# Kernel optimization log

Measured on AMD Instinct MI355X. Metric: run time of the kernel, lower is better.

## Reference

```python
import jax, jax.numpy as jnp
import numpy as np

TAU = 20.0        # LIFNeuron default tau
THRESHOLD = 1.0   # LIFNeuron default threshold
RESET = 0.0       # LIFNeuron default reset
DT = 1.0          # SpikingNeuralNetwork dt
ALPHA = DT / TAU

B, T, I, H, O = 256, 128, 512, 1024, 512


def setup_inputs() -> dict:
    key = jax.random.key(0)
    ks = jax.random.split(key, 6)
    def w(k, shape, fan_in):
        return (jax.random.normal(k, shape, jnp.float32) / np.sqrt(fan_in)).astype(jnp.float32)
    return {
        "x":  jax.random.normal(ks[0], (B, T, I), jnp.float32),
        "We": w(ks[1], (I, H), I), "be": jnp.zeros((H,), jnp.float32),
        "W1": w(ks[2], (H, H), H), "b1": jnp.zeros((H,), jnp.float32),
        "W2": w(ks[3], (H, H), H), "b2": jnp.zeros((H,), jnp.float32),
        "Wo": w(ks[4], (H, O), H), "bo": jnp.zeros((O,), jnp.float32),
    }


def _lif(v, inp):
    # v += (-v + inp) * dt/tau; spike = (v >= thr); v = v*(1-spike) + reset*spike
    v = v + (inp - v) * ALPHA
    spike = (v >= THRESHOLD).astype(v.dtype)
    v = v * (1.0 - spike) + RESET * spike
    return v, spike


def reference(x, We, be, W1, b1, W2, b2, Wo, bo):
    b, t, _ = x.shape
    h_dim = We.shape[1]
    o_dim = Wo.shape[1]

    def step(carry, xt):
        v1, v2, vo = carry
        h = jax.nn.relu(xt @ We + be)          # [B, H]
        v1, s1 = _lif(v1, h)                   # neuron 0 (only 2 of 3 neurons used: zip truncation)
        h = s1 @ W1 + b1
        v2, s2 = _lif(v2, h)                   # neuron 1
        h = s2 @ W2 + b2                       # last hidden layer: no neuron applied before output_layer
        vo, so = _lif(vo, h @ Wo + bo)         # output neuron
        return (v1, v2, vo), (s1, s2, so)

    init = (jnp.zeros((b, h_dim), x.dtype),
            jnp.zeros((b, h_dim), x.dtype),
            jnp.zeros((b, o_dim), x.dtype))
    _, (S1, S2, SO) = jax.lax.scan(step, init, jnp.swapaxes(x, 0, 1))  # time-major scan
    # output_spike at last timestep + full (detached) spike history, stacked over time
    return SO[-1], S1, S2, SO
```

## Files before the change

### kernel.cpp

```cpp
#include <hip/hip_runtime.h>
#include <cstdint>
#include <cstddef>

#define B_ 256
#define T_ 128
#define I_ 512
#define H_ 1024
#define O_ 512
static constexpr float ALPHA = 1.0f / 20.0f;
static constexpr float THR   = 1.0f;
static constexpr float S12   = 0.000244140625f;

typedef _Float16 f16;
typedef __attribute__((ext_vector_type(8))) _Float16 f16x8;
typedef __attribute__((ext_vector_type(4))) float f32x4;

template<bool PERM_X, bool RELU>
__global__ __launch_bounds__(256)
void gemm128(const float* __restrict__ A, const float* __restrict__ Bw,
             const float* __restrict__ bias, float* __restrict__ C,
             int M, int N, int K) {
    constexpr int BM = 128, BN = 128, BK = 16, TM = 8, TN = 8;
    __shared__ float As[BK][BM];
    __shared__ float Bs[BK][BN + 4];

    const int tid = threadIdx.x;
    const int ntile = N / BN;
    const int bx = blockIdx.x % ntile;
    const int by = blockIdx.x / ntile;
    const int row0 = by * BM, col0 = bx * BN;
    const int tx = tid & 15;
    const int ty = tid >> 4;

    float acc[TM][TN] = {};

    for (int k0 = 0; k0 < K; k0 += BK) {
#pragma unroll
        for (int p = 0; p < 2; ++p) {
            int f = tid + p * 256;
            int r  = f >> 2;
            int kc = (f & 3) << 2;
            int m = row0 + r;
            const float* arow;
            if (PERM_X) {
                int t = m >> 8;
                int b = m & 255;
                arow = A + (size_t)(b * T_ + t) * K;
            } else {
                arow = A + (size_t)m * K;
            }
            float4 v = *reinterpret_cast<const float4*>(arow + k0 + kc);
            As[kc + 0][r] = v.x;
            As[kc + 1][r] = v.y;
            As[kc + 2][r] = v.z;
            As[kc + 3][r] = v.w;
        }
#pragma unroll
        for (int p = 0; p < 2; ++p) {
            int f = tid + p * 256;
            int r  = f >> 5;
            int nc = (f & 31) << 2;
            float4 v = *reinterpret_cast<const float4*>(Bw + (size_t)(k0 + r) * N + col0 + nc);
            *reinterpret_cast<float4*>(&Bs[r][nc]) = v;
        }
        __syncthreads();

#pragma unroll
        for (int k = 0; k < BK; ++k) {
            float a[TM], b[TN];
#pragma unroll
            for (int i = 0; i < TM; ++i) a[i] = As[k][ty * TM + i];
#pragma unroll
            for (int j = 0; j < TN; ++j) b[j] = Bs[k][tx * TN + j];
#pragma unroll
            for (int i = 0; i < TM; ++i)
#pragma unroll
                for (int j = 0; j < TN; ++j)
                    acc[i][j] += a[i] * b[j];
        }
        __syncthreads();
    }

#pragma unroll
    for (int i = 0; i < TM; ++i) {
        size_t m = (size_t)(row0 + ty * TM + i);
#pragma unroll
        for (int jj = 0; jj < TN; jj += 4) {
            int n = col0 + tx * TN + jj;
            float4 c4;
            float c0 = acc[i][jj + 0] + bias[n + 0];
            float c1 = acc[i][jj + 1] + bias[n + 1];
            float c2 = acc[i][jj + 2] + bias[n + 2];
            float c3 = acc[i][jj + 3] + bias[n + 3];
            if (RELU) {
                c0 = fmaxf(c0, 0.f); c1 = fmaxf(c1, 0.f);
                c2 = fmaxf(c2, 0.f); c3 = fmaxf(c3, 0.f);
            }
            c4.x = c0; c4.y = c1; c4.z = c2; c4.w = c3;
            *reinterpret_cast<float4*>(C + m * N + n) = c4;
        }
    }
}

__device__ inline void gload_lds16(const void* gsrc, void* ldsdst) {
    __builtin_amdgcn_global_load_lds(
        (const __attribute__((address_space(1))) unsigned int*)gsrc,
        (__attribute__((address_space(3))) unsigned int*)ldsdst, 16, 0, 0);
}

template<bool SPLITX, bool PERM, bool RELU, bool WRITE_LAST>
__global__ __launch_bounds__(256, 2)
void gemm_lif(const float* __restrict__ A,
              const f16* __restrict__ Bhi,
              const f16* __restrict__ Blo,
              const float* __restrict__ bias,
              float* __restrict__ S,
              float* __restrict__ last_out,
              int N, int K) {
    constexpr int BK = 32;
    constexpr int NBUF = SPLITX ? 4 : 3;
    constexpr int BUFSTR = NBUF * 4096;
    constexpr size_t SMEM = (2 * BUFSTR * 2 > 64 * 132 * 4)
                                ? (size_t)(2 * BUFSTR * 2)
                                : (size_t)(64 * 132 * 4);
    __shared__ __align__(16) char smem[SMEM];
    f16* sm = (f16*)smem;
    float (*Cs)[132] = (float (*)[132])smem;

    const int tid  = threadIdx.x;
    const int lane = tid & 63;
    const int w    = tid >> 6;
    const int wr   = w >> 1, wc = w & 1;
    const int ntile = N >> 7;
    const int bx = blockIdx.x % ntile;
    const int b  = blockIdx.x / ntile;
    const int col0 = bx << 7;

    f32x4 acc0[4][4], acc1[4][4];
#pragma unroll
    for (int mi = 0; mi < 4; ++mi)
#pragma unroll
        for (int ni = 0; ni < 4; ++ni) {
            acc0[mi][ni] = {0.f, 0.f, 0.f, 0.f};
            acc1[mi][ni] = {0.f, 0.f, 0.f, 0.f};
        }

    {
        f16* Ah0 = sm;
        f16* Bh0 = sm + 4096;
        f16* Bl0 = sm + 8192;
        f16* Al0 = sm + 12288;
#pragma unroll
        for (int p = 0; p < 2; ++p) {
            int chunk = w * 2 + p;
            int r  = chunk * 16 + (lane >> 2);
            int kq = lane & 3;
            size_t off = (size_t)(col0 + r) * K + kq * 8;
            gload_lds16(Bhi + off, Bh0 + chunk * 512);
            gload_lds16(Blo + off, Bl0 + chunk * 512);
        }
#pragma unroll
        for (int p = 0; p < 4; ++p) {
            int c = tid + p * 256;
            int r = c >> 3;
            int q = c & 7;
            const float* arow = PERM ? A + (size_t)(b * T_ + r) * K
                                     : A + (size_t)(r * B_ + b) * K;
            float4 v = *reinterpret_cast<const float4*>(arow + q * 4);
            union { f16 h[4]; uint2 u; } hi;
            hi.h[0] = (f16)v.x; hi.h[1] = (f16)v.y;
            hi.h[2] = (f16)v.z; hi.h[3] = (f16)v.w;
            *reinterpret_cast<uint2*>(&Ah0[r * BK + q * 4]) = hi.u;
            if (SPLITX) {
                union { f16 h[4]; uint2 u; } lo;
                lo.h[0] = (f16)((v.x - (float)hi.h[0]) * 4096.0f);
                lo.h[1] = (f16)((v.y - (float)hi.h[1]) * 4096.0f);
                lo.h[2] = (f16)((v.z - (float)hi.h[2]) * 4096.0f);
                lo.h[3] = (f16)((v.w - (float)hi.h[3]) * 4096.0f);
                *reinterpret_cast<uint2*>(&Al0[r * BK + q * 4]) = lo.u;
            }
        }
    }
    __syncthreads();

    const int NIT = K / BK;
    for (int it = 0; it < NIT; ++it) {
        const int cur = it & 1, nxt = cur ^ 1;
        const bool more = (it + 1 < NIT);
        const int k0n = (it + 1) * BK;

        f16* Ah_c = sm + cur * BUFSTR;
        f16* Bh_c = Ah_c + 4096;
        f16* Bl_c = Ah_c + 8192;
        f16* Al_c = Ah_c + 12288;
        f16* Ah_n = sm + nxt * BUFSTR;
        f16* Bh_n = Ah_n + 4096;
        f16* Bl_n = Ah_n + 8192;
        f16* Al_n = Ah_n + 12288;

        float4 a4[4];
        if (more) {
#pragma unroll
            for (int p = 0; p < 2; ++p) {
                int chunk = w * 2 + p;
                int r  = chunk * 16 + (lane >> 2);
                int kq = lane & 3;
                size_t off = (size_t)(col0 + r) * K + k0n + kq * 8;
                gload_lds16(Bhi + off, Bh_n + chunk * 512);
                gload_lds16(Blo + off, Bl_n + chunk * 512);
            }
#pragma unroll
            for (int p = 0; p < 4; ++p) {
                int c = tid + p * 256;
                int r = c >> 3;
                int q = c & 7;
                const float* arow = PERM ? A + (size_t)(b * T_ + r) * K
                                         : A + (size_t)(r * B_ + b) * K;
                a4[p] = *reinterpret_cast<const float4*>(arow + k0n + q * 4);
            }
        }

        {
            f16x8 ahi[4], alo[4];
#pragma unroll
            for (int mi = 0; mi < 4; ++mi) {
                int ar = (wr * 64 + mi * 16 + (lane & 15)) * BK + (lane >> 4) * 8;
                ahi[mi] = *reinterpret_cast<const f16x8*>(&Ah_c[ar]);
                if (SPLITX) alo[mi] = *reinterpret_cast<const f16x8*>(&Al_c[ar]);
            }
#pragma unroll
            for (int ni = 0; ni < 4; ++ni) {
                int br = (wc * 64 + ni * 16 + (lane & 15)) * BK + (lane >> 4) * 8;
                f16x8 bh = *reinterpret_cast<const f16x8*>(&Bh_c[br]);
                f16x8 bl = *reinterpret_cast<const f16x8*>(&Bl_c[br]);
#pragma unroll
                for (int mi = 0; mi < 4; ++mi) {
                    acc0[mi][ni] = __builtin_amdgcn_mfma_f32_16x16x32_f16(
                        ahi[mi], bh, acc0[mi][ni], 0, 0, 0);
                    acc1[mi][ni] = __builtin_amdgcn_mfma_f32_16x16x32_f16(
                        ahi[mi], bl, acc1[mi][ni], 0, 0, 0);
                    if (SPLITX)
                        acc1[mi][ni] = __builtin_amdgcn_mfma_f32_16x16x32_f16(
                            alo[mi], bh, acc1[mi][ni], 0, 0, 0);
                }
            }
        }

        if (more) {
#pragma unroll
            for (int p = 0; p < 4; ++p) {
                int c = tid + p * 256;
                int r = c >> 3;
                int q = c & 7;
                float4 v = a4[p];
                union { f16 h[4]; uint2 u; } hi;
                hi.h[0] = (f16)v.x; hi.h[1] = (f16)v.y;
                hi.h[2] = (f16)v.z; hi.h[3] = (f16)v.w;
                *reinterpret_cast<uint2*>(&Ah_n[r * BK + q * 4]) = hi.u;
                if (SPLITX) {
                    union { f16 h[4]; uint2 u; } lo;
                    lo.h[0] = (f16)((v.x - (float)hi.h[0]) * 4096.0f);
                    lo.h[1] = (f16)((v.y - (float)hi.h[1]) * 4096.0f);
                    lo.h[2] = (f16)((v.z - (float)hi.h[2]) * 4096.0f);
                    lo.h[3] = (f16)((v.w - (float)hi.h[3]) * 4096.0f);
                    *reinterpret_cast<uint2*>(&Al_n[r * BK + q * 4]) = lo.u;
                }
            }
        }
        __syncthreads();
    }

    float v = 0.f, s = 0.f;
    float* Sp = S + (size_t)b * N + col0 + (tid & 127);
    const size_t tstride = (size_t)B_ * N;

    if (wr == 0) {
#pragma unroll
        for (int ni = 0; ni < 4; ++ni) {
            int col = wc * 64 + ni * 16 + (lane & 15);
            float bv = bias[col0 + col];
#pragma unroll
            for (int mi = 0; mi < 4; ++mi) {
                int rowb = mi * 16 + ((lane >> 4) << 2);
#pragma unroll
                for (int r = 0; r < 4; ++r) {
                    float cv = acc0[mi][ni][r] + S12 * acc1[mi][ni][r] + bv;
                    if (RELU) cv = fmaxf(cv, 0.f);
                    Cs[rowb + r][col] = cv;
                }
            }
        }
    }
    __syncthreads();
    if (tid < 128) {
#pragma unroll 4
        for (int t = 0; t < 64; ++t) {
            float in = Cs[t][tid];
            v = v + (in - v) * ALPHA;
            bool sp = (v >= THR);
            s = sp ? 1.0f : 0.0f;
            Sp[(size_t)t * tstride] = s;
            v = sp ? 0.0f : v;
        }
    }
    __syncthreads();
    if (wr == 1) {
#pragma unroll
        for (int ni = 0; ni < 4; ++ni) {
            int col = wc * 64 + ni * 16 + (lane & 15);
            float bv = bias[col0 + col];
#pragma unroll
            for (int mi = 0; mi < 4; ++mi) {
                int rowb = mi * 16 + ((lane >> 4) << 2);
#pragma unroll
                for (int r = 0; r < 4; ++r) {
                    float cv = acc0[mi][ni][r] + S12 * acc1[mi][ni][r] + bv;
                    if (RELU) cv = fmaxf(cv, 0.f);
                    Cs[rowb + r][col] = cv;
                }
            }
        }
    }
    __syncthreads();
    if (tid < 128) {
#pragma unroll 4
        for (int t = 64; t < 128; ++t) {
            float in = Cs[t - 64][tid];
            v = v + (in - v) * ALPHA;
            bool sp = (v >= THR);
            s = sp ? 1.0f : 0.0f;
            Sp[(size_t)t * tstride] = s;
            v = sp ? 0.0f : v;
        }
        if (WRITE_LAST) last_out[(size_t)b * N + col0 + tid] = s;
    }
}

__global__ __launch_bounds__(256)
void lif_scan(float* __restrict__ buf, int BH, float* __restrict__ last_out) {
    int j = blockIdx.x * 256 + threadIdx.x;
    if (j >= BH) return;
    float v = 0.f;
    float last = 0.f;
    for (int t = 0; t < T_; ++t) {
        size_t idx = (size_t)t * BH + j;
        float in = buf[idx];
        v = v + (in - v) * ALPHA;
        bool sp = (v >= THR);
        last = sp ? 1.0f : 0.0f;
        buf[idx] = last;
        v = sp ? 0.0f : v;
    }
    if (last_out) last_out[j] = last;
}

__global__ __launch_bounds__(256)
void make_wf2(const float* __restrict__ W2, const float* __restrict__ Wo,
              float* __restrict__ Wf) {
    __shared__ float w2s[64][33];
    __shared__ float wos[64][68];
    const int tid = threadIdx.x;
    const int ht = blockIdx.x >> 3, ot = blockIdx.x & 7;
    const int h0 = ht * 32, o0 = ot * 64;
    const int th = tid >> 3;
    const int to = tid & 7;

    double acc[8] = {0, 0, 0, 0, 0, 0, 0, 0};

    for (int k0 = 0; k0 < H_; k0 += 64) {
#pragma unroll
        for (int p = 0; p < 2; ++p) {
            int f = tid + p * 256;
            int i = f >> 4;
            int j4 = (f & 15) << 2;
            float4 v = *reinterpret_cast<const float4*>(
                W2 + (size_t)(h0 + i) * H_ + k0 + j4);
            w2s[j4 + 0][i] = v.x; w2s[j4 + 1][i] = v.y;
            w2s[j4 + 2][i] = v.z; w2s[j4 + 3][i] = v.w;
        }
#pragma unroll
        for (int p = 0; p < 4; ++p) {
            int f = tid + p * 256;
            int r = f >> 4;
            int c4 = (f & 15) << 2;
            float4 v = *reinterpret_cast<const float4*>(
                Wo + (size_t)(k0 + r) * O_ + o0 + c4);
            wos[r][c4 + 0] = v.x; wos[r][c4 + 1] = v.y;
            wos[r][c4 + 2] = v.z; wos[r][c4 + 3] = v.w;
        }
        __syncthreads();

#pragma unroll 8
        for (int k = 0; k < 64; ++k) {
            double a = (double)w2s[k][th];
#pragma unroll
            for (int j = 0; j < 8; ++j)
                acc[j] += a * (double)wos[k][to * 8 + j];
        }
        __syncthreads();
    }
#pragma unroll
    for (int j = 0; j < 8; ++j)
        Wf[(size_t)(h0 + th) * O_ + o0 + to * 8 + j] = (float)acc[j];
}

__global__ __launch_bounds__(256)
void make_bf(const float* __restrict__ Wo, const float* __restrict__ b2,
             const float* __restrict__ bo, float* __restrict__ bf) {
    int o = blockIdx.x * 256 + threadIdx.x;
    if (o >= O_) return;
    double acc = (double)bo[o];
    for (int h = 0; h < H_; ++h)
        acc += (double)b2[h] * (double)Wo[(size_t)h * O_ + o];
    bf[o] = (float)acc;
}

__global__ __launch_bounds__(256)
void split_w16(const float* __restrict__ W, f16* __restrict__ hi,
               f16* __restrict__ lo, int K, int N) {
    int idx = blockIdx.x * 256 + threadIdx.x;
    if (idx >= K * N) return;
    int n = idx / K;
    int k = idx - n * K;
    float wv = W[(size_t)k * N + n];
    f16 h0 = (f16)wv;
    float r = (wv - (float)h0) * 4096.0f;
    f16 h1 = (f16)r;
    hi[idx] = h0; lo[idx] = h1;
}

extern "C" void kernel_launch(void* const* d_in, const int* in_sizes, int n_in,
                              void* d_out, int out_size, void* d_ws, size_t ws_size,
                              hipStream_t stream) {
    const float* x  = (const float*)d_in[0];
    const float* We = (const float*)d_in[1];
    const float* be = (const float*)d_in[2];
    const float* W1 = (const float*)d_in[3];
    const float* b1 = (const float*)d_in[4];
    const float* W2 = (const float*)d_in[5];
    const float* b2 = (const float*)d_in[6];
    const float* Wo = (const float*)d_in[7];
    const float* bo = (const float*)d_in[8];

    float* out = (float*)d_out;
    float* so_last = out;
    float* S1 = out + (size_t)B_ * O_;
    float* S2 = S1 + (size_t)T_ * B_ * H_;
    float* SO = S2 + (size_t)T_ * B_ * H_;

    const int TB = T_ * B_;
    dim3 blk(256);

    const size_t sz_we  = (size_t)I_ * H_ * 2;
    const size_t sz_w1  = (size_t)H_ * H_ * 2;
    const size_t sz_wf  = (size_t)H_ * O_ * 2;
    const size_t off_weh = 0;
    const size_t off_wel = off_weh + sz_we;
    const size_t off_w1h = off_wel + sz_we;
    const size_t off_w1l = off_w1h + sz_w1;
    const size_t off_wf32 = off_w1l + sz_w1;
    const size_t off_bf   = off_wf32 + (size_t)H_ * O_ * 4;
    const size_t off_wfh  = off_bf + (size_t)O_ * 4;
    const size_t off_wfl  = off_wfh + sz_wf;
    const size_t need     = off_wfl + sz_wf;

    if (ws_size >= need) {
        char* ws = (char*)d_ws;
        f16*   weh = (f16*)(ws + off_weh);
        f16*   wel = (f16*)(ws + off_wel);
        f16*   w1h = (f16*)(ws + off_w1h);
        f16*   w1l = (f16*)(ws + off_w1l);
        float* Wf  = (float*)(ws + off_wf32);
        float* bf  = (float*)(ws + off_bf);
        f16*   wfh = (f16*)(ws + off_wfh);
        f16*   wfl = (f16*)(ws + off_wfl);

        split_w16<<<dim3((I_ * H_ + 255) / 256), blk, 0, stream>>>(We, weh, wel, I_, H_);
        split_w16<<<dim3((H_ * H_ + 255) / 256), blk, 0, stream>>>(W1, w1h, w1l, H_, H_);
        make_wf2<<<dim3(256), blk, 0, stream>>>(W2, Wo, Wf);
        make_bf<<<dim3(2), blk, 0, stream>>>(Wo, b2, bo, bf);
        split_w16<<<dim3((H_ * O_ + 255) / 256), blk, 0, stream>>>(Wf, wfh, wfl, H_, O_);

        gemm_lif<true, true, true, false><<<dim3(B_ * (H_ / 128)), blk, 0, stream>>>(
            x, weh, wel, be, S1, nullptr, H_, I_);

        gemm_lif<false, false, false, false><<<dim3(B_ * (H_ / 128)), blk, 0, stream>>>(
            S1, w1h, w1l, b1, S2, nullptr, H_, H_);

        gemm_lif<false, false, false, true><<<dim3(B_ * (O_ / 128)), blk, 0, stream>>>(
            S2, wfh, wfl, bf, SO, so_last, O_, H_);
    } else {
        float* Wf = (float*)d_ws;
        float* bf = Wf + (size_t)H_ * O_;
        gemm128<true, true><<<dim3((TB / 128) * (H_ / 128)), blk, 0, stream>>>(
            x, We, be, S1, TB, H_, I_);
        lif_scan<<<dim3((B_ * H_ + 255) / 256), blk, 0, stream>>>(S1, B_ * H_, nullptr);
        gemm128<false, false><<<dim3((TB / 128) * (H_ / 128)), blk, 0, stream>>>(
            S1, W1, b1, S2, TB, H_, H_);
        lif_scan<<<dim3((B_ * H_ + 255) / 256), blk, 0, stream>>>(S2, B_ * H_, nullptr);
        make_wf2<<<dim3(256), blk, 0, stream>>>(W2, Wo, Wf);
        make_bf<<<dim3(2), blk, 0, stream>>>(Wo, b2, bo, bf);
        gemm128<false, false><<<dim3((TB / 128) * (O_ / 128)), blk, 0, stream>>>(
            S2, Wf, bf, SO, TB, O_, H_);
        lif_scan<<<dim3((B_ * O_ + 255) / 256), blk, 0, stream>>>(SO, B_ * O_, so_last);
    }
}
```

Measured before the change: 644.3 us.

## Pack spike outputs into bitmasks and feed packed spikes to later GEMMs

The first and second LIF GEMM kernels now also write each timestep's spikes as ballot bitmasks into a packed workspace buffer. The following GEMM reads these 1-bit spikes and expands them to f16 in registers instead of loading fp32 spike tensors, and it drops the low-part A MFMA because spikes are exactly 0/1 in f16. Weight splits are pre-swizzled so direct global-to-LDS loads land in a bank-conflict-free layout, and blocks are remapped to group batches. This adds extra ballot stores and more workspace use, and the new path is taken only when the workspace is large enough.

```diff
diff --git a/kernel.cpp b/kernel.cpp
--- a/kernel.cpp
+++ b/kernel.cpp
@@ -14,6 +14,12 @@
 typedef _Float16 f16;
 typedef __attribute__((ext_vector_type(8))) _Float16 f16x8;
 typedef __attribute__((ext_vector_type(4))) float f32x4;
+
+__device__ inline void gload_lds16(const void* gsrc, void* ldsdst) {
+    __builtin_amdgcn_global_load_lds(
+        (const __attribute__((address_space(1))) unsigned int*)gsrc,
+        (__attribute__((address_space(3))) unsigned int*)ldsdst, 16, 0, 0);
+}
 
 template<bool PERM_X, bool RELU>
 __global__ __launch_bounds__(256)
@@ -102,20 +108,12 @@
     }
 }
 
-__device__ inline void gload_lds16(const void* gsrc, void* ldsdst) {
-    __builtin_amdgcn_global_load_lds(
-        (const __attribute__((address_space(1))) unsigned int*)gsrc,
-        (__attribute__((address_space(3))) unsigned int*)ldsdst, 16, 0, 0);
-}
-
 template<bool SPLITX, bool PERM, bool RELU, bool WRITE_LAST>
 __global__ __launch_bounds__(256, 2)
 void gemm_lif(const float* __restrict__ A,
-              const f16* __restrict__ Bhi,
-              const f16* __restrict__ Blo,
+              const f16* __restrict__ Bhi, const f16* __restrict__ Blo,
               const float* __restrict__ bias,
-              float* __restrict__ S,
-              float* __restrict__ last_out,
+              float* __restrict__ S, float* __restrict__ last_out,
               int N, int K) {
     constexpr int BK = 32;
     constexpr int NBUF = SPLITX ? 4 : 3;
@@ -336,6 +334,408 @@
     }
 }
 
+__global__ __launch_bounds__(256, 2)
+void gemm_lif_x(const float* __restrict__ A,
+                const f16* __restrict__ Bhi, const f16* __restrict__ Blo,
+                const float* __restrict__ bias,
+                float* __restrict__ S,
+                uint32_t* __restrict__ Pk,
+                int N, int K) {
+    constexpr int BK = 32;
+    constexpr int BUFSTR = 4 * 4096;
+    __shared__ __align__(16) char smem[2 * BUFSTR * 2];
+    f16* sm = (f16*)smem;
+    float (*Cs)[132] = (float (*)[132])smem;
+
+    const int tid  = threadIdx.x;
+    const int lane = tid & 63;
+    const int w    = tid >> 6;
+    const int wr   = w >> 1, wc = w & 1;
+    const int nt   = N >> 7;
+    const int ls   = 31 - __builtin_clz(nt);
+    const int jj_  = blockIdx.x >> 3;
+    const int bx   = jj_ & (nt - 1);
+    const int b    = ((blockIdx.x & 7) << 5) + (jj_ >> ls);
+    const int col0 = bx << 7;
+    const int sw = (((lane >> 4) ^ ((lane >> 1) & 3)) << 3);
+
+    f32x4 acc0[4][4], acc1[4][4];
+#pragma unroll
+    for (int mi = 0; mi < 4; ++mi)
+#pragma unroll
+        for (int ni = 0; ni < 4; ++ni) {
+            acc0[mi][ni] = {0.f, 0.f, 0.f, 0.f};
+            acc1[mi][ni] = {0.f, 0.f, 0.f, 0.f};
+        }
+
+    {
+        f16* Ah0 = sm;
+        f16* Bh0 = sm + 4096;
+        f16* Bl0 = sm + 8192;
+        f16* Al0 = sm + 12288;
+#pragma unroll
+        for (int p = 0; p < 2; ++p) {
+            int chunk = w * 2 + p;
+            int r  = chunk * 16 + (lane >> 2);
+            int kq = lane & 3;
+            size_t off = (size_t)(col0 + r) * K + kq * 8;
+            gload_lds16(Bhi + off, Bh0 + chunk * 512);
+            gload_lds16(Blo + off, Bl0 + chunk * 512);
+        }
+#pragma unroll
+        for (int p = 0; p < 4; ++p) {
+            int c = tid + p * 256;
+            int r = c >> 3;
+            int q = c & 7;
+            const float* arow = A + (size_t)(b * T_ + r) * K;
+            float4 v = *reinterpret_cast<const float4*>(arow + q * 4);
+            int aoff = r * 32 + ((((q >> 1) ^ ((r >> 1) & 3))) << 3) + ((q & 1) << 2);
+            union { f16 h[4]; uint2 u; } hi;
+            hi.h[0] = (f16)v.x; hi.h[1] = (f16)v.y;
+            hi.h[2] = (f16)v.z; hi.h[3] = (f16)v.w;
+            *reinterpret_cast<uint2*>(&Ah0[aoff]) = hi.u;
+            union { f16 h[4]; uint2 u; } lo;
+            lo.h[0] = (f16)((v.x - (float)hi.h[0]) * 4096.0f);
+            lo.h[1] = (f16)((v.y - (float)hi.h[1]) * 4096.0f);
+            lo.h[2] = (f16)((v.z - (float)hi.h[2]) * 4096.0f);
+            lo.h[3] = (f16)((v.w - (float)hi.h[3]) * 4096.0f);
+            *reinterpret_cast<uint2*>(&Al0[aoff]) = lo.u;
+        }
+    }
+    __syncthreads();
+
+    const int NIT = K / BK;
+    for (int it = 0; it < NIT; ++it) {
+        const int cur = it & 1, nxt = cur ^ 1;
+        const bool more = (it + 1 < NIT);
+        const int k0n = (it + 1) * BK;
+
+        f16* Ah_c = sm + cur * BUFSTR;
+        f16* Bh_c = Ah_c + 4096;
+        f16* Bl_c = Ah_c + 8192;
+        f16* Al_c = Ah_c + 12288;
+        f16* Ah_n = sm + nxt * BUFSTR;
+        f16* Bh_n = Ah_n + 4096;
+        f16* Bl_n = Ah_n + 8192;
+        f16* Al_n = Ah_n + 12288;
+
+        float4 a4[4];
+        if (more) {
+#pragma unroll
+            for (int p = 0; p < 2; ++p) {
+                int chunk = w * 2 + p;
+                int r  = chunk * 16 + (lane >> 2);
+                int kq = lane & 3;
+                size_t off = (size_t)(col0 + r) * K + k0n + kq * 8;
+                gload_lds16(Bhi + off, Bh_n + chunk * 512);
+                gload_lds16(Blo + off, Bl_n + chunk * 512);
+            }
+#pragma unroll
+            for (int p = 0; p < 4; ++p) {
+                int c = tid + p * 256;
+                int r = c >> 3;
+                int q = c & 7;
+                const float* arow = A + (size_t)(b * T_ + r) * K;
+                a4[p] = *reinterpret_cast<const float4*>(arow + k0n + q * 4);
+            }
+        }
+
+        {
+            f16x8 ahi[4], alo[4];
+#pragma unroll
+            for (int mi = 0; mi < 4; ++mi) {
+                int ar = (wr * 64 + mi * 16 + (lane & 15)) * 32 + sw;
+                ahi[mi] = *reinterpret_cast<const f16x8*>(&Ah_c[ar]);
+                alo[mi] = *reinterpret_cast<const f16x8*>(&Al_c[ar]);
+            }
+#pragma unroll
+            for (int ni = 0; ni < 4; ++ni) {
+                int br = (wc * 64 + ni * 16 + (lane & 15)) * 32 + sw;
+                f16x8 bh = *reinterpret_cast<const f16x8*>(&Bh_c[br]);
+                f16x8 bl = *reinterpret_cast<const f16x8*>(&Bl_c[br]);
+#pragma unroll
+                for (int mi = 0; mi < 4; ++mi) {
+                    acc0[mi][ni] = __builtin_amdgcn_mfma_f32_16x16x32_f16(
+                        ahi[mi], bh, acc0[mi][ni], 0, 0, 0);
+                    acc1[mi][ni] = __builtin_amdgcn_mfma_f32_16x16x32_f16(
+                        ahi[mi], bl, acc1[mi][ni], 0, 0, 0);
+                    acc1[mi][ni] = __builtin_amdgcn_mfma_f32_16x16x32_f16(
+                        alo[mi], bh, acc1[mi][ni], 0, 0, 0);
+                }
+            }
+        }
+
+        if (more) {
+#pragma unroll
+            for (int p = 0; p < 4; ++p) {
+                int c = tid + p * 256;
+                int r = c >> 3;
+                int q = c & 7;
+                float4 v = a4[p];
+                int aoff = r * 32 + ((((q >> 1) ^ ((r >> 1) & 3))) << 3) + ((q & 1) << 2);
+                union { f16 h[4]; uint2 u; } hi;
+                hi.h[0] = (f16)v.x; hi.h[1] = (f16)v.y;
+                hi.h[2] = (f16)v.z; hi.h[3] = (f16)v.w;
+                *reinterpret_cast<uint2*>(&Ah_n[aoff]) = hi.u;
+                union { f16 h[4]; uint2 u; } lo;
+                lo.h[0] = (f16)((v.x - (float)hi.h[0]) * 4096.0f);
+                lo.h[1] = (f16)((v.y - (float)hi.h[1]) * 4096.0f);
+                lo.h[2] = (f16)((v.z - (float)hi.h[2]) * 4096.0f);
+                lo.h[3] = (f16)((v.w - (float)hi.h[3]) * 4096.0f);
+                *reinterpret_cast<uint2*>(&Al_n[aoff]) = lo.u;
+            }
+        }
+        __syncthreads();
+    }
+
+    float v = 0.f;
+    float* Sp = S + (size_t)b * N + col0 + (tid & 127);
+    const size_t tstride = (size_t)B_ * N;
+    const int PkW = N >> 5;
+    const size_t pkbase = (size_t)(col0 >> 5) + ((tid >> 6) << 1);
+
+    if (wr == 0) {
+#pragma unroll
+        for (int ni = 0; ni < 4; ++ni) {
+            int col = wc * 64 + ni * 16 + (lane & 15);
+            float bv = bias[col0 + col];
+#pragma unroll
+            for (int mi = 0; mi < 4; ++mi) {
+                int rowb = mi * 16 + ((lane >> 4) << 2);
+#pragma unroll
+                for (int r = 0; r < 4; ++r) {
+                    float cv = fmaxf(acc0[mi][ni][r] + S12 * acc1[mi][ni][r] + bv, 0.f);
+                    Cs[rowb + r][col] = cv;
+                }
+            }
+        }
+    }
+    __syncthreads();
+    if (tid < 128) {
+#pragma unroll 4
+        for (int t = 0; t < 64; ++t) {
+            float in = Cs[t][tid];
+            v = v + (in - v) * ALPHA;
+            bool sp = (v >= THR);
+            Sp[(size_t)t * tstride] = sp ? 1.0f : 0.0f;
+            v = sp ? 0.0f : v;
+            unsigned long long bm = __ballot(sp);
+            if (lane == 0)
+                *reinterpret_cast<unsigned long long*>(
+                    &Pk[((size_t)t * B_ + b) * PkW + pkbase]) = bm;
+        }
+    }
+    __syncthreads();
+    if (wr == 1) {
+#pragma unroll
+        for (int ni = 0; ni < 4; ++ni) {
+            int col = wc * 64 + ni * 16 + (lane & 15);
+            float bv = bias[col0 + col];
+#pragma unroll
+            for (int mi = 0; mi < 4; ++mi) {
+                int rowb = mi * 16 + ((lane >> 4) << 2);
+#pragma unroll
+                for (int r = 0; r < 4; ++r) {
+                    float cv = fmaxf(acc0[mi][ni][r] + S12 * acc1[mi][ni][r] + bv, 0.f);
+                    Cs[rowb + r][col] = cv;
+                }
+            }
+        }
+    }
+    __syncthreads();
+    if (tid < 128) {
+#pragma unroll 4
+        for (int t = 64; t < 128; ++t) {
+            float in = Cs[t - 64][tid];
+            v = v + (in - v) * ALPHA;
+            bool sp = (v >= THR);
+            Sp[(size_t)t * tstride] = sp ? 1.0f : 0.0f;
+            v = sp ? 0.0f : v;
+            unsigned long long bm = __ballot(sp);
+            if (lane == 0)
+                *reinterpret_cast<unsigned long long*>(
+                    &Pk[((size_t)t * B_ + b) * PkW + pkbase]) = bm;
+        }
+    }
+}
+
+template<bool WRITE_LAST, bool PACK_OUT>
+__global__ __launch_bounds__(256, 2)
+void gemm_lif_pk(const uint32_t* __restrict__ Apk,
+                 const f16* __restrict__ Bhi, const f16* __restrict__ Blo,
+                 const float* __restrict__ bias,
+                 float* __restrict__ S,
+                 float* __restrict__ last_out,
+                 uint32_t* __restrict__ Pk_out,
+                 int N, int K) {
+    __shared__ __align__(16) char smem[64 * 132 * 4];
+    f16* sm = (f16*)smem;
+    float (*Cs)[132] = (float (*)[132])smem;
+
+    const int tid  = threadIdx.x;
+    const int lane = tid & 63;
+    const int w    = tid >> 6;
+    const int wr   = w >> 1, wc = w & 1;
+    const int nt   = N >> 7;
+    const int ls   = 31 - __builtin_clz(nt);
+    const int jj_  = blockIdx.x >> 3;
+    const int bx   = jj_ & (nt - 1);
+    const int b    = ((blockIdx.x & 7) << 5) + (jj_ >> ls);
+    const int col0 = bx << 7;
+    const int sw = (((lane >> 4) ^ ((lane >> 1) & 3)) << 3);
+    const int PkW = K >> 5;
+    const int sh  = (lane >> 4) << 3;
+
+    size_t arow[4];
+#pragma unroll
+    for (int mi = 0; mi < 4; ++mi) {
+        int r = wr * 64 + mi * 16 + (lane & 15);
+        arow[mi] = ((size_t)r * B_ + b) * PkW;
+    }
+
+    f32x4 acc0[4][4], acc1[4][4];
+#pragma unroll
+    for (int mi = 0; mi < 4; ++mi)
+#pragma unroll
+        for (int ni = 0; ni < 4; ++ni) {
+            acc0[mi][ni] = {0.f, 0.f, 0.f, 0.f};
+            acc1[mi][ni] = {0.f, 0.f, 0.f, 0.f};
+        }
+
+    {
+#pragma unroll
+        for (int p = 0; p < 2; ++p) {
+            int chunk = w * 2 + p;
+            int r  = chunk * 16 + (lane >> 2);
+            int kq = lane & 3;
+            size_t off = (size_t)(col0 + r) * K + kq * 8;
+            gload_lds16(Bhi + off, sm + chunk * 512);
+            gload_lds16(Blo + off, sm + 4096 + chunk * 512);
+        }
+    }
+    __syncthreads();
+
+    const int NIT = K / 32;
+    for (int it = 0; it < NIT; ++it) {
+        const int cur = it & 1, nxt = cur ^ 1;
+        f16* Bh_c = sm + cur * 8192;
+        f16* Bl_c = Bh_c + 4096;
+        if (it + 1 < NIT) {
+            f16* Bh_n = sm + nxt * 8192;
+            f16* Bl_n = Bh_n + 4096;
+            int k0n = (it + 1) * 32;
+#pragma unroll
+            for (int p = 0; p < 2; ++p) {
+                int chunk = w * 2 + p;
+                int r  = chunk * 16 + (lane >> 2);
+                int kq = lane & 3;
+                size_t off = (size_t)(col0 + r) * K + k0n + kq * 8;
+                gload_lds16(Bhi + off, Bh_n + chunk * 512);
+                gload_lds16(Blo + off, Bl_n + chunk * 512);
+            }
+        }
+
+        f16x8 af[4];
+#pragma unroll
+        for (int mi = 0; mi < 4; ++mi) {
+            uint32_t mm = Apk[arow[mi] + it] >> sh;
+            union { f16 h[8]; f16x8 v; } au;
+#pragma unroll
+            for (int j = 0; j < 8; ++j)
+                au.h[j] = ((mm >> j) & 1) ? (f16)1.0f : (f16)0.0f;
+            af[mi] = au.v;
+        }
+
+#pragma unroll
+        for (int ni = 0; ni < 4; ++ni) {
+            int br = (wc * 64 + ni * 16 + (lane & 15)) * 32 + sw;
+            f16x8 bh = *reinterpret_cast<const f16x8*>(&Bh_c[br]);
+            f16x8 bl = *reinterpret_cast<const f16x8*>(&Bl_c[br]);
+#pragma unroll
+            for (int mi = 0; mi < 4; ++mi) {
+                acc0[mi][ni] = __builtin_amdgcn_mfma_f32_16x16x32_f16(
+                    af[mi], bh, acc0[mi][ni], 0, 0, 0);
+                acc1[mi][ni] = __builtin_amdgcn_mfma_f32_16x16x32_f16(
+                    af[mi], bl, acc1[mi][ni], 0, 0, 0);
+            }
+        }
+        __syncthreads();
+    }
+
+    float v = 0.f, s = 0.f;
+    float* Sp = S + (size_t)b * N + col0 + (tid & 127);
+    const size_t tstride = (size_t)B_ * N;
+    const int PkWo = N >> 5;
+    const size_t pkbase = (size_t)(col0 >> 5) + ((tid >> 6) << 1);
+
+    if (wr == 0) {
+#pragma unroll
+        for (int ni = 0; ni < 4; ++ni) {
+            int col = wc * 64 + ni * 16 + (lane & 15);
+            float bv = bias[col0 + col];
+#pragma unroll
+            for (int mi = 0; mi < 4; ++mi) {
+                int rowb = mi * 16 + ((lane >> 4) << 2);
+#pragma unroll
+                for (int r = 0; r < 4; ++r)
+                    Cs[rowb + r][col] = acc0[mi][ni][r] + S12 * acc1[mi][ni][r] + bv;
+            }
+        }
+    }
+    __syncthreads();
+    if (tid < 128) {
+#pragma unroll 4
+        for (int t = 0; t < 64; ++t) {
+            float in = Cs[t][tid];
+            v = v + (in - v) * ALPHA;
+            bool sp = (v >= THR);
+            s = sp ? 1.0f : 0.0f;
+            Sp[(size_t)t * tstride] = s;
+            v = sp ? 0.0f : v;
+            if (PACK_OUT) {
+                unsigned long long bm = __ballot(sp);
+                if (lane == 0)
+                    *reinterpret_cast<unsigned long long*>(
+                        &Pk_out[((size_t)t * B_ + b) * PkWo + pkbase]) = bm;
+            }
+        }
+    }
+    __syncthreads();
+    if (wr == 1) {
+#pragma unroll
+        for (int ni = 0; ni < 4; ++ni) {
+            int col = wc * 64 + ni * 16 + (lane & 15);
+            float bv = bias[col0 + col];
+#pragma unroll
+            for (int mi = 0; mi < 4; ++mi) {
+                int rowb = mi * 16 + ((lane >> 4) << 2);
+#pragma unroll
+                for (int r = 0; r < 4; ++r)
+                    Cs[rowb + r][col] = acc0[mi][ni][r] + S12 * acc1[mi][ni][r] + bv;
+            }
+        }
+    }
+    __syncthreads();
+    if (tid < 128) {
+#pragma unroll 4
+        for (int t = 64; t < 128; ++t) {
+            float in = Cs[t - 64][tid];
+            v = v + (in - v) * ALPHA;
+            bool sp = (v >= THR);
+            s = sp ? 1.0f : 0.0f;
+            Sp[(size_t)t * tstride] = s;
+            v = sp ? 0.0f : v;
+            if (PACK_OUT) {
+                unsigned long long bm = __ballot(sp);
+                if (lane == 0)
+                    *reinterpret_cast<unsigned long long*>(
+                        &Pk_out[((size_t)t * B_ + b) * PkWo + pkbase]) = bm;
+            }
+        }
+        if (WRITE_LAST) last_out[(size_t)b * N + col0 + tid] = s;
+    }
+}
+
 __global__ __launch_bounds__(256)
 void lif_scan(float* __restrict__ buf, int BH, float* __restrict__ last_out) {
     int j = blockIdx.x * 256 + threadIdx.x;
@@ -415,13 +815,16 @@
     bf[o] = (float)acc;
 }
 
+template<bool SWZ>
 __global__ __launch_bounds__(256)
 void split_w16(const float* __restrict__ W, f16* __restrict__ hi,
                f16* __restrict__ lo, int K, int N) {
     int idx = blockIdx.x * 256 + threadIdx.x;
     if (idx >= K * N) return;
     int n = idx / K;
-    int k = idx - n * K;
+    int ks = idx - n * K;
+    int k = SWZ ? ((ks & ~31) | ((((ks >> 3) & 3) ^ ((n >> 1) & 3)) << 3) | (ks & 7))
+                : ks;
     float wv = W[(size_t)k * N + n];
     f16 h0 = (f16)wv;
     float r = (wv - (float)h0) * 4096.0f;
@@ -451,42 +854,76 @@
     const int TB = T_ * B_;
     dim3 blk(256);
 
-    const size_t sz_we  = (size_t)I_ * H_ * 2;
-    const size_t sz_w1  = (size_t)H_ * H_ * 2;
-    const size_t sz_wf  = (size_t)H_ * O_ * 2;
+    const size_t MB = 1024 * 1024;
     const size_t off_weh = 0;
-    const size_t off_wel = off_weh + sz_we;
-    const size_t off_w1h = off_wel + sz_we;
-    const size_t off_w1l = off_w1h + sz_w1;
-    const size_t off_wf32 = off_w1l + sz_w1;
-    const size_t off_bf   = off_wf32 + (size_t)H_ * O_ * 4;
-    const size_t off_wfh  = off_bf + (size_t)O_ * 4;
-    const size_t off_wfl  = off_wfh + sz_wf;
-    const size_t need     = off_wfl + sz_wf;
-
-    if (ws_size >= need) {
+    const size_t off_wel = 1 * MB;
+    const size_t off_w1h = 2 * MB;
+    const size_t off_w1l = 4 * MB;
+    const size_t off_wfh = 6 * MB;
+    const size_t off_wfl = 7 * MB;
+    const size_t off_bf  = 8 * MB;
+    const size_t off_D   = 8 * MB + 4096;
+    const size_t off_pk2 = off_D + 4 * MB;
+    const size_t need3   = off_pk2 + 4 * MB;
+
+    const size_t m_off_weh = 0;
+    const size_t m_off_wel = m_off_weh + (size_t)I_ * H_ * 2;
+    const size_t m_off_w1h = m_off_wel + (size_t)I_ * H_ * 2;
+    const size_t m_off_w1l = m_off_w1h + (size_t)H_ * H_ * 2;
+    const size_t m_off_wf32 = m_off_w1l + (size_t)H_ * H_ * 2;
+    const size_t m_off_bf   = m_off_wf32 + (size_t)H_ * O_ * 4;
+    const size_t m_off_wfh  = m_off_bf + (size_t)O_ * 4;
+    const size_t m_off_wfl  = m_off_wfh + (size_t)H_ * O_ * 2;
+    const size_t need2      = m_off_wfl + (size_t)H_ * O_ * 2;
+
+    if (ws_size >= need3) {
         char* ws = (char*)d_ws;
         f16*   weh = (f16*)(ws + off_weh);
         f16*   wel = (f16*)(ws + off_wel);
         f16*   w1h = (f16*)(ws + off_w1h);
         f16*   w1l = (f16*)(ws + off_w1l);
-        float* Wf  = (float*)(ws + off_wf32);
-        float* bf  = (float*)(ws + off_bf);
         f16*   wfh = (f16*)(ws + off_wfh);
         f16*   wfl = (f16*)(ws + off_wfl);
-
-        split_w16<<<dim3((I_ * H_ + 255) / 256), blk, 0, stream>>>(We, weh, wel, I_, H_);
-        split_w16<<<dim3((H_ * H_ + 255) / 256), blk, 0, stream>>>(W1, w1h, w1l, H_, H_);
+        float* bf  = (float*)(ws + off_bf);
+        float* Wf  = (float*)(ws + off_D);
+        uint32_t* pk1 = (uint32_t*)(ws + off_D);
+        uint32_t* pk2 = (uint32_t*)(ws + off_pk2);
+
+        split_w16<true><<<dim3((I_ * H_ + 255) / 256), blk, 0, stream>>>(We, weh, wel, I_, H_);
+        split_w16<true><<<dim3((H_ * H_ + 255) / 256), blk, 0, stream>>>(W1, w1h, w1l, H_, H_);
         make_wf2<<<dim3(256), blk, 0, stream>>>(W2, Wo, Wf);
         make_bf<<<dim3(2), blk, 0, stream>>>(Wo, b2, bo, bf);
-        split_w16<<<dim3((H_ * O_ + 255) / 256), blk, 0, stream>>>(Wf, wfh, wfl, H_, O_);
+        split_w16<true><<<dim3((H_ * O_ + 255) / 256), blk, 0, stream>>>(Wf, wfh, wfl, H_, O_);
+
+        gemm_lif_x<<<dim3(B_ * (H_ / 128)), blk, 0, stream>>>(
+            x, weh, wel, be, S1, pk1, H_, I_);
+
+        gemm_lif_pk<false, true><<<dim3(B_ * (H_ / 128)), blk, 0, stream>>>(
+            pk1, w1h, w1l, b1, S2, nullptr, pk2, H_, H_);
+
+        gemm_lif_pk<true, false><<<dim3(B_ * (O_ / 128)), blk, 0, stream>>>(
+            pk2, wfh, wfl, bf, SO, so_last, nullptr, O_, H_);
+    } else if (ws_size >= need2) {
+        char* ws = (char*)d_ws;
+        f16*   weh = (f16*)(ws + m_off_weh);
+        f16*   wel = (f16*)(ws + m_off_wel);
+        f16*   w1h = (f16*)(ws + m_off_w1h);
+        f16*   w1l = (f16*)(ws + m_off_w1l);
+        float* Wf  = (float*)(ws + m_off_wf32);
+        float* bf  = (float*)(ws + m_off_bf);
+        f16*   wfh = (f16*)(ws + m_off_wfh);
+        f16*   wfl = (f16*)(ws + m_off_wfl);
+
+        split_w16<false><<<dim3((I_ * H_ + 255) / 256), blk, 0, stream>>>(We, weh, wel, I_, H_);
+        split_w16<false><<<dim3((H_ * H_ + 255) / 256), blk, 0, stream>>>(W1, w1h, w1l, H_, H_);
+        make_wf2<<<dim3(256), blk, 0, stream>>>(W2, Wo, Wf);
+        make_bf<<<dim3(2), blk, 0, stream>>>(Wo, b2, bo, bf);
+        split_w16<false><<<dim3((H_ * O_ + 255) / 256), blk, 0, stream>>>(Wf, wfh, wfl, H_, O_);
 
         gemm_lif<true, true, true, false><<<dim3(B_ * (H_ / 128)), blk, 0, stream>>>(
             x, weh, wel, be, S1, nullptr, H_, I_);
-
         gemm_lif<false, false, false, false><<<dim3(B_ * (H_ / 128)), blk, 0, stream>>>(
             S1, w1h, w1l, b1, S2, nullptr, H_, H_);
-
         gemm_lif<false, false, false, true><<<dim3(B_ * (O_ / 128)), blk, 0, stream>>>(
             S2, wfh, wfl, bf, SO, so_last, O_, H_);
     } else {
```

New measurement: 657.0 us. No clear change (+2.0%).

## Emit f16 spike copies and consume them in dedicated f16-A GEMM-LIF kernels

Applied to the files above, without the earlier changes.

The first two GEMM-LIF stages now also write their spike outputs as f16 into a batch-major workspace buffer. A new gemm_lif_h kernel loads these f16 spikes directly via global-to-LDS loads with an XOR swizzle, and the weight split kernel swizzles k to match. This avoids re-reading fp32 spikes and converting A on the fly in the second and third GEMMs. The cost is extra f16 writes of 64 MB per stage, a larger workspace requirement, and a fallback path when the workspace is too small.

```diff
diff --git a/kernel.cpp b/kernel.cpp
--- a/kernel.cpp
+++ b/kernel.cpp
@@ -14,6 +14,12 @@
 typedef _Float16 f16;
 typedef __attribute__((ext_vector_type(8))) _Float16 f16x8;
 typedef __attribute__((ext_vector_type(4))) float f32x4;
+
+__device__ inline void gload_lds16(const void* gsrc, void* ldsdst) {
+    __builtin_amdgcn_global_load_lds(
+        (const __attribute__((address_space(1))) unsigned int*)gsrc,
+        (__attribute__((address_space(3))) unsigned int*)ldsdst, 16, 0, 0);
+}
 
 template<bool PERM_X, bool RELU>
 __global__ __launch_bounds__(256)
@@ -102,20 +108,13 @@
     }
 }
 
-__device__ inline void gload_lds16(const void* gsrc, void* ldsdst) {
-    __builtin_amdgcn_global_load_lds(
-        (const __attribute__((address_space(1))) unsigned int*)gsrc,
-        (__attribute__((address_space(3))) unsigned int*)ldsdst, 16, 0, 0);
-}
-
-template<bool SPLITX, bool PERM, bool RELU, bool WRITE_LAST>
+template<bool SPLITX, bool PERM, bool RELU, bool WRITE_LAST, bool F16OUT>
 __global__ __launch_bounds__(256, 2)
 void gemm_lif(const float* __restrict__ A,
-              const f16* __restrict__ Bhi,
-              const f16* __restrict__ Blo,
+              const f16* __restrict__ Bhi, const f16* __restrict__ Blo,
               const float* __restrict__ bias,
-              float* __restrict__ S,
-              float* __restrict__ last_out,
+              float* __restrict__ S, float* __restrict__ last_out,
+              f16* __restrict__ Sf,
               int N, int K) {
     constexpr int BK = 32;
     constexpr int NBUF = SPLITX ? 4 : 3;
@@ -300,6 +299,7 @@
             bool sp = (v >= THR);
             s = sp ? 1.0f : 0.0f;
             Sp[(size_t)t * tstride] = s;
+            if (F16OUT) Sf[((size_t)b * T_ + t) * N + col0 + tid] = (f16)s;
             v = sp ? 0.0f : v;
         }
     }
@@ -330,6 +330,163 @@
             bool sp = (v >= THR);
             s = sp ? 1.0f : 0.0f;
             Sp[(size_t)t * tstride] = s;
+            if (F16OUT) Sf[((size_t)b * T_ + t) * N + col0 + tid] = (f16)s;
+            v = sp ? 0.0f : v;
+        }
+        if (WRITE_LAST) last_out[(size_t)b * N + col0 + tid] = s;
+    }
+}
+
+template<bool WRITE_LAST, bool F16OUT>
+__global__ __launch_bounds__(256, 2)
+void gemm_lif_h(const f16* __restrict__ Af,
+                const f16* __restrict__ Bhi,
+                const f16* __restrict__ Blo,
+                const float* __restrict__ bias,
+                float* __restrict__ S,
+                float* __restrict__ last_out,
+                f16* __restrict__ Sf,
+                int N, int K) {
+    constexpr int BK = 32;
+    constexpr int BUFF = 3 * 4096;
+    __shared__ __align__(16) char smem[2 * BUFF * 2];
+    f16* sm = (f16*)smem;
+    float (*Cs)[132] = (float (*)[132])smem;
+
+    const int tid  = threadIdx.x;
+    const int lane = tid & 63;
+    const int w    = tid >> 6;
+    const int wr   = w >> 1, wc = w & 1;
+    const int ntile = N >> 7;
+    const int bx = blockIdx.x % ntile;
+    const int b  = blockIdx.x / ntile;
+    const int col0 = bx << 7;
+    const int sw = (((lane >> 4) ^ ((lane >> 1) & 3)) << 3);
+
+    f32x4 acc0[4][4], acc1[4][4];
+#pragma unroll
+    for (int mi = 0; mi < 4; ++mi)
+#pragma unroll
+        for (int ni = 0; ni < 4; ++ni) {
+            acc0[mi][ni] = {0.f, 0.f, 0.f, 0.f};
+            acc1[mi][ni] = {0.f, 0.f, 0.f, 0.f};
+        }
+
+    const int r0   = (w * 2 + 0) * 16 + (lane >> 2);
+    const int r1   = (w * 2 + 1) * 16 + (lane >> 2);
+    const int kqs  = lane & 3;
+    const int kqa0 = kqs ^ ((r0 >> 1) & 3);
+    const int kqa1 = kqs ^ ((r1 >> 1) & 3);
+
+    {
+        size_t b0 = (size_t)(col0 + r0) * K + kqs * 8;
+        size_t b1 = (size_t)(col0 + r1) * K + kqs * 8;
+        size_t a0 = ((size_t)b * T_ + r0) * K + kqa0 * 8;
+        size_t a1 = ((size_t)b * T_ + r1) * K + kqa1 * 8;
+        gload_lds16(Af + a0,  sm + (w * 2 + 0) * 512);
+        gload_lds16(Af + a1,  sm + (w * 2 + 1) * 512);
+        gload_lds16(Bhi + b0, sm + 4096 + (w * 2 + 0) * 512);
+        gload_lds16(Bhi + b1, sm + 4096 + (w * 2 + 1) * 512);
+        gload_lds16(Blo + b0, sm + 8192 + (w * 2 + 0) * 512);
+        gload_lds16(Blo + b1, sm + 8192 + (w * 2 + 1) * 512);
+    }
+    __syncthreads();
+
+    const int NIT = K / BK;
+    for (int it = 0; it < NIT; ++it) {
+        f16* cur = sm + (it & 1) * BUFF;
+        if (it + 1 < NIT) {
+            f16* nb = sm + ((it + 1) & 1) * BUFF;
+            int k0n = (it + 1) * BK;
+            size_t b0 = (size_t)(col0 + r0) * K + k0n + kqs * 8;
+            size_t b1 = (size_t)(col0 + r1) * K + k0n + kqs * 8;
+            size_t a0 = ((size_t)b * T_ + r0) * K + k0n + kqa0 * 8;
+            size_t a1 = ((size_t)b * T_ + r1) * K + k0n + kqa1 * 8;
+            gload_lds16(Af + a0,  nb + (w * 2 + 0) * 512);
+            gload_lds16(Af + a1,  nb + (w * 2 + 1) * 512);
+            gload_lds16(Bhi + b0, nb + 4096 + (w * 2 + 0) * 512);
+            gload_lds16(Bhi + b1, nb + 4096 + (w * 2 + 1) * 512);
+            gload_lds16(Blo + b0, nb + 8192 + (w * 2 + 0) * 512);
+            gload_lds16(Blo + b1, nb + 8192 + (w * 2 + 1) * 512);
+        }
+
+        f16x8 af[4];
+#pragma unroll
+        for (int mi = 0; mi < 4; ++mi)
+            af[mi] = *reinterpret_cast<const f16x8*>(
+                &cur[(wr * 64 + mi * 16 + (lane & 15)) * BK + sw]);
+#pragma unroll
+        for (int ni = 0; ni < 4; ++ni) {
+            int br = (wc * 64 + ni * 16 + (lane & 15)) * BK + sw;
+            f16x8 bh = *reinterpret_cast<const f16x8*>(&cur[4096 + br]);
+            f16x8 bl = *reinterpret_cast<const f16x8*>(&cur[8192 + br]);
+#pragma unroll
+            for (int mi = 0; mi < 4; ++mi) {
+                acc0[mi][ni] = __builtin_amdgcn_mfma_f32_16x16x32_f16(
+                    af[mi], bh, acc0[mi][ni], 0, 0, 0);
+                acc1[mi][ni] = __builtin_amdgcn_mfma_f32_16x16x32_f16(
+                    af[mi], bl, acc1[mi][ni], 0, 0, 0);
+            }
+        }
+        __syncthreads();
+    }
+
+    float v = 0.f, s = 0.f;
+    float* Sp = S + (size_t)b * N + col0 + (tid & 127);
+    const size_t tstride = (size_t)B_ * N;
+
+    if (wr == 0) {
+#pragma unroll
+        for (int ni = 0; ni < 4; ++ni) {
+            int col = wc * 64 + ni * 16 + (lane & 15);
+            float bv = bias[col0 + col];
+#pragma unroll
+            for (int mi = 0; mi < 4; ++mi) {
+                int rowb = mi * 16 + ((lane >> 4) << 2);
+#pragma unroll
+                for (int r = 0; r < 4; ++r)
+                    Cs[rowb + r][col] = acc0[mi][ni][r] + S12 * acc1[mi][ni][r] + bv;
+            }
+        }
+    }
+    __syncthreads();
+    if (tid < 128) {
+#pragma unroll 4
+        for (int t = 0; t < 64; ++t) {
+            float in = Cs[t][tid];
+            v = v + (in - v) * ALPHA;
+            bool sp = (v >= THR);
+            s = sp ? 1.0f : 0.0f;
+            Sp[(size_t)t * tstride] = s;
+            if (F16OUT) Sf[((size_t)b * T_ + t) * N + col0 + tid] = (f16)s;
+            v = sp ? 0.0f : v;
+        }
+    }
+    __syncthreads();
+    if (wr == 1) {
+#pragma unroll
+        for (int ni = 0; ni < 4; ++ni) {
+            int col = wc * 64 + ni * 16 + (lane & 15);
+            float bv = bias[col0 + col];
+#pragma unroll
+            for (int mi = 0; mi < 4; ++mi) {
+                int rowb = mi * 16 + ((lane >> 4) << 2);
+#pragma unroll
+                for (int r = 0; r < 4; ++r)
+                    Cs[rowb + r][col] = acc0[mi][ni][r] + S12 * acc1[mi][ni][r] + bv;
+            }
+        }
+    }
+    __syncthreads();
+    if (tid < 128) {
+#pragma unroll 4
+        for (int t = 64; t < 128; ++t) {
+            float in = Cs[t - 64][tid];
+            v = v + (in - v) * ALPHA;
+            bool sp = (v >= THR);
+            s = sp ? 1.0f : 0.0f;
+            Sp[(size_t)t * tstride] = s;
+            if (F16OUT) Sf[((size_t)b * T_ + t) * N + col0 + tid] = (f16)s;
             v = sp ? 0.0f : v;
         }
         if (WRITE_LAST) last_out[(size_t)b * N + col0 + tid] = s;
@@ -415,13 +572,16 @@
     bf[o] = (float)acc;
 }
 
+template<bool SWZ>
 __global__ __launch_bounds__(256)
 void split_w16(const float* __restrict__ W, f16* __restrict__ hi,
                f16* __restrict__ lo, int K, int N) {
     int idx = blockIdx.x * 256 + threadIdx.x;
     if (idx >= K * N) return;
     int n = idx / K;
-    int k = idx - n * K;
+    int ks = idx - n * K;
+    int k = SWZ ? ((ks & ~31) | ((((ks >> 3) & 3) ^ ((n >> 1) & 3)) << 3) | (ks & 7))
+                : ks;
     float wv = W[(size_t)k * N + n];
     f16 h0 = (f16)wv;
     float r = (wv - (float)h0) * 4096.0f;
@@ -451,44 +611,80 @@
     const int TB = T_ * B_;
     dim3 blk(256);
 
-    const size_t sz_we  = (size_t)I_ * H_ * 2;
-    const size_t sz_w1  = (size_t)H_ * H_ * 2;
-    const size_t sz_wf  = (size_t)H_ * O_ * 2;
+    const size_t MB = 1024 * 1024;
     const size_t off_weh = 0;
-    const size_t off_wel = off_weh + sz_we;
-    const size_t off_w1h = off_wel + sz_we;
-    const size_t off_w1l = off_w1h + sz_w1;
-    const size_t off_wf32 = off_w1l + sz_w1;
-    const size_t off_bf   = off_wf32 + (size_t)H_ * O_ * 4;
-    const size_t off_wfh  = off_bf + (size_t)O_ * 4;
-    const size_t off_wfl  = off_wfh + sz_wf;
-    const size_t need     = off_wfl + sz_wf;
-
-    if (ws_size >= need) {
+    const size_t off_wel = 1 * MB;
+    const size_t off_w1h = 2 * MB;
+    const size_t off_w1l = 4 * MB;
+    const size_t off_wfh = 6 * MB;
+    const size_t off_wfl = 7 * MB;
+    const size_t off_bf  = 8 * MB;
+    const size_t off_wf  = 8 * MB + 4096;
+    const size_t off_s1f = 10 * MB + 4096;
+    const size_t sz_s1f  = (size_t)T_ * B_ * H_ * 2;
+    const size_t off_s2f = off_s1f + sz_s1f;
+    const size_t need_hi = off_s2f + sz_s1f;
+
+    const size_t m_off_weh = 0;
+    const size_t m_off_wel = m_off_weh + (size_t)I_ * H_ * 2;
+    const size_t m_off_w1h = m_off_wel + (size_t)I_ * H_ * 2;
+    const size_t m_off_w1l = m_off_w1h + (size_t)H_ * H_ * 2;
+    const size_t m_off_wf32 = m_off_w1l + (size_t)H_ * H_ * 2;
+    const size_t m_off_bf   = m_off_wf32 + (size_t)H_ * O_ * 4;
+    const size_t m_off_wfh  = m_off_bf + (size_t)O_ * 4;
+    const size_t m_off_wfl  = m_off_wfh + (size_t)H_ * O_ * 2;
+    const size_t need_mid   = m_off_wfl + (size_t)H_ * O_ * 2;
+
+    if (ws_size >= need_hi) {
         char* ws = (char*)d_ws;
         f16*   weh = (f16*)(ws + off_weh);
         f16*   wel = (f16*)(ws + off_wel);
         f16*   w1h = (f16*)(ws + off_w1h);
         f16*   w1l = (f16*)(ws + off_w1l);
-        float* Wf  = (float*)(ws + off_wf32);
-        float* bf  = (float*)(ws + off_bf);
         f16*   wfh = (f16*)(ws + off_wfh);
         f16*   wfl = (f16*)(ws + off_wfl);
-
-        split_w16<<<dim3((I_ * H_ + 255) / 256), blk, 0, stream>>>(We, weh, wel, I_, H_);
-        split_w16<<<dim3((H_ * H_ + 255) / 256), blk, 0, stream>>>(W1, w1h, w1l, H_, H_);
+        float* bf  = (float*)(ws + off_bf);
+        float* Wf  = (float*)(ws + off_wf);
+        f16*   s1f = (f16*)(ws + off_s1f);
+        f16*   s2f = (f16*)(ws + off_s2f);
+
+        split_w16<false><<<dim3((I_ * H_ + 255) / 256), blk, 0, stream>>>(We, weh, wel, I_, H_);
+        split_w16<true ><<<dim3((H_ * H_ + 255) / 256), blk, 0, stream>>>(W1, w1h, w1l, H_, H_);
         make_wf2<<<dim3(256), blk, 0, stream>>>(W2, Wo, Wf);
         make_bf<<<dim3(2), blk, 0, stream>>>(Wo, b2, bo, bf);
-        split_w16<<<dim3((H_ * O_ + 255) / 256), blk, 0, stream>>>(Wf, wfh, wfl, H_, O_);
-
-        gemm_lif<true, true, true, false><<<dim3(B_ * (H_ / 128)), blk, 0, stream>>>(
-            x, weh, wel, be, S1, nullptr, H_, I_);
-
-        gemm_lif<false, false, false, false><<<dim3(B_ * (H_ / 128)), blk, 0, stream>>>(
-            S1, w1h, w1l, b1, S2, nullptr, H_, H_);
-
-        gemm_lif<false, false, false, true><<<dim3(B_ * (O_ / 128)), blk, 0, stream>>>(
-            S2, wfh, wfl, bf, SO, so_last, O_, H_);
+        split_w16<true ><<<dim3((H_ * O_ + 255) / 256), blk, 0, stream>>>(Wf, wfh, wfl, H_, O_);
+
+        gemm_lif<true, true, true, false, true><<<dim3(B_ * (H_ / 128)), blk, 0, stream>>>(
+            x, weh, wel, be, S1, nullptr, s1f, H_, I_);
+
+        gemm_lif_h<false, true><<<dim3(B_ * (H_ / 128)), blk, 0, stream>>>(
+            s1f, w1h, w1l, b1, S2, nullptr, s2f, H_, H_);
+
+        gemm_lif_h<true, false><<<dim3(B_ * (O_ / 128)), blk, 0, stream>>>(
+            s2f, wfh, wfl, bf, SO, so_last, nullptr, O_, H_);
+    } else if (ws_size >= need_mid) {
+        char* ws = (char*)d_ws;
+        f16*   weh = (f16*)(ws + m_off_weh);
+        f16*   wel = (f16*)(ws + m_off_wel);
+        f16*   w1h = (f16*)(ws + m_off_w1h);
+        f16*   w1l = (f16*)(ws + m_off_w1l);
+        float* Wf  = (float*)(ws + m_off_wf32);
+        float* bf  = (float*)(ws + m_off_bf);
+        f16*   wfh = (f16*)(ws + m_off_wfh);
+        f16*   wfl = (f16*)(ws + m_off_wfl);
+
+        split_w16<false><<<dim3((I_ * H_ + 255) / 256), blk, 0, stream>>>(We, weh, wel, I_, H_);
+        split_w16<false><<<dim3((H_ * H_ + 255) / 256), blk, 0, stream>>>(W1, w1h, w1l, H_, H_);
+        make_wf2<<<dim3(256), blk, 0, stream>>>(W2, Wo, Wf);
+        make_bf<<<dim3(2), blk, 0, stream>>>(Wo, b2, bo, bf);
+        split_w16<false><<<dim3((H_ * O_ + 255) / 256), blk, 0, stream>>>(Wf, wfh, wfl, H_, O_);
+
+        gemm_lif<true, true, true, false, false><<<dim3(B_ * (H_ / 128)), blk, 0, stream>>>(
+            x, weh, wel, be, S1, nullptr, nullptr, H_, I_);
+        gemm_lif<false, false, false, false, false><<<dim3(B_ * (H_ / 128)), blk, 0, stream>>>(
+            S1, w1h, w1l, b1, S2, nullptr, nullptr, H_, H_);
+        gemm_lif<false, false, false, true, false><<<dim3(B_ * (O_ / 128)), blk, 0, stream>>>(
+            S2, wfh, wfl, bf, SO, so_last, nullptr, O_, H_);
     } else {
         float* Wf = (float*)d_ws;
         float* bf = Wf + (size_t)H_ * O_;
```

Measured after the change: 582.2 us. 9.6% less time.
